# Performance work log

Hardware: AMD Instinct MI355X
Metric: run time of the kernel (lower is better)

Reference implementation:

```python
import jax, jax.numpy as jnp
import numpy as np

BATCH, N_IN, N_MID, N_OUT = 1048576, 64, 32, 10


def setup_inputs() -> dict:
    key = jax.random.key(0)
    k_x, k_w1, k_b1, k_w2, k_b2 = jax.random.split(key, 5)
    # scalar synapse weights k collectively form dense matrices; init like
    # Synapse.init_weight: uniform(-sqrt(1/fan_in), sqrt(1/fan_in))
    v1 = np.sqrt(1.0 / N_IN)
    v2 = np.sqrt(1.0 / N_MID)
    return {
        "x": jax.random.normal(k_x, (BATCH, N_IN), dtype=jnp.float32),
        "W1": jax.random.uniform(k_w1, (N_IN, N_MID), dtype=jnp.float32, minval=-v1, maxval=v1),
        "b1": jnp.zeros((N_MID,), dtype=jnp.float32),  # obtain_float_parameter inits to 0.0
        "W2": jax.random.uniform(k_w2, (N_MID, N_OUT), dtype=jnp.float32, minval=-v2, maxval=v2),
        "b2": jnp.zeros((N_OUT,), dtype=jnp.float32),
    }


def reference(x, W1, b1, W2, b2):
    # RegularNeuron: output = ReLU(b + sum_j k_j * input_j)  -> relu(x @ W1 + b1)
    h = jax.nn.relu(x @ W1 + b1)  # [batch, n_middle]
    # DestinationNeuron (no activation): y = b + sum_j k_j * h_j -> h @ W2 + b2
    y = h @ W2 + b2  # [batch, n_outputs]
    return y
```

## Files before the change

### kernel.cpp

```cpp
#include <hip/hip_runtime.h>


#define N_IN  64
#define N_MID 32
#define N_OUT 10

#define WAVES_PER_BLOCK 4
#define TILES_PER_WAVE  4
#define ROWS_PER_TILE   16
#define ROWS_PER_BLOCK  (WAVES_PER_BLOCK * TILES_PER_WAVE * ROWS_PER_TILE)
#define H_STRIDE        80

typedef short bf16x8 __attribute__((ext_vector_type(8)));
typedef float f32x4  __attribute__((ext_vector_type(4)));

static __device__ __forceinline__ short f2bf(float f) {
    __bf16 h = (__bf16)f;
    return __builtin_bit_cast(short, h);
}

static __device__ __forceinline__ unsigned pk2bf(float lo, float hi) {
    unsigned l = (unsigned short)__builtin_bit_cast(unsigned short, (__bf16)lo);
    unsigned h = (unsigned short)__builtin_bit_cast(unsigned short, (__bf16)hi);
    return (h << 16) | l;
}

__global__ __launch_bounds__(256)
void livenet_mfma(const float* __restrict__ x,
                  const float* __restrict__ W1,
                  const float* __restrict__ b1,
                  const float* __restrict__ W2,
                  const float* __restrict__ b2,
                  float* __restrict__ out,
                  int batch) {
    __shared__ unsigned char h_lds_all[WAVES_PER_BLOCK][ROWS_PER_TILE * H_STRIDE];

    const int lane = threadIdx.x & 63;
    const int wave = threadIdx.x >> 6;
    const int g    = lane >> 4;
    const int c    = lane & 15;

    unsigned char* h_lds = h_lds_all[wave];

    bf16x8 w1f[2][2];
    #pragma unroll
    for (int n = 0; n < 2; ++n)
        #pragma unroll
        for (int p = 0; p < 2; ++p)
            #pragma unroll
            for (int i = 0; i < 8; ++i) {
                int k = p * 32 + 8 * g + i;
                w1f[n][p][i] = f2bf(W1[k * N_MID + n * 16 + c]);
            }

    bf16x8 w2f;
    #pragma unroll
    for (int i = 0; i < 8; ++i) {
        int kpos = 8 * g + i;
        int col  = (kpos & 1) * 16 + (kpos >> 1);
        w2f[i] = (c < N_OUT) ? f2bf(W2[col * N_OUT + c]) : (short)0;
    }

    const float b1v0 = b1[c];
    const float b1v1 = b1[16 + c];
    const float b2v  = (c < N_OUT) ? b2[c] : 0.0f;

    const size_t wave_row0 = (size_t)blockIdx.x * ROWS_PER_BLOCK
                           + (size_t)wave * (TILES_PER_WAVE * ROWS_PER_TILE);
    const bool full = (wave_row0 + TILES_PER_WAVE * ROWS_PER_TILE) <= (size_t)batch;

    const float* xbase = x + (wave_row0 + (size_t)c) * N_IN + 8 * g;

    if (full) {
        float4 v0 = *(const float4*)(xbase + 0);
        float4 v1 = *(const float4*)(xbase + 4);
        float4 v2 = *(const float4*)(xbase + 32);
        float4 v3 = *(const float4*)(xbase + 36);

        #pragma unroll
        for (int t = 0; t < TILES_PER_WAVE; ++t) {
            float4 n0 = v0, n1 = v1, n2 = v2, n3 = v3;
            if (t + 1 < TILES_PER_WAVE) {
                const float* xp = xbase + (size_t)(t + 1) * ROWS_PER_TILE * N_IN;
                n0 = *(const float4*)(xp + 0);
                n1 = *(const float4*)(xp + 4);
                n2 = *(const float4*)(xp + 32);
                n3 = *(const float4*)(xp + 36);
            }

            bf16x8 a0, a1;
            a0[0] = f2bf(v0.x); a0[1] = f2bf(v0.y); a0[2] = f2bf(v0.z); a0[3] = f2bf(v0.w);
            a0[4] = f2bf(v1.x); a0[5] = f2bf(v1.y); a0[6] = f2bf(v1.z); a0[7] = f2bf(v1.w);
            a1[0] = f2bf(v2.x); a1[1] = f2bf(v2.y); a1[2] = f2bf(v2.z); a1[3] = f2bf(v2.w);
            a1[4] = f2bf(v3.x); a1[5] = f2bf(v3.y); a1[6] = f2bf(v3.z); a1[7] = f2bf(v3.w);

            f32x4 acc0 = {b1v0, b1v0, b1v0, b1v0};
            f32x4 acc1 = {b1v1, b1v1, b1v1, b1v1};
            acc0 = __builtin_amdgcn_mfma_f32_16x16x32_bf16(a0, w1f[0][0], acc0, 0, 0, 0);
            acc0 = __builtin_amdgcn_mfma_f32_16x16x32_bf16(a1, w1f[0][1], acc0, 0, 0, 0);
            acc1 = __builtin_amdgcn_mfma_f32_16x16x32_bf16(a0, w1f[1][0], acc1, 0, 0, 0);
            acc1 = __builtin_amdgcn_mfma_f32_16x16x32_bf16(a1, w1f[1][1], acc1, 0, 0, 0);

            #pragma unroll
            for (int r = 0; r < 4; ++r) {
                const int rowr = 4 * g + r;
                *(unsigned*)(h_lds + rowr * H_STRIDE + 4 * c) =
                    pk2bf(fmaxf(acc0[r], 0.0f), fmaxf(acc1[r], 0.0f));
            }
            __asm__ volatile("" ::: "memory");

            const bf16x8 hfrag = *(const bf16x8*)(h_lds + c * H_STRIDE + 16 * g);
            f32x4 acc2 = {b2v, b2v, b2v, b2v};
            acc2 = __builtin_amdgcn_mfma_f32_16x16x32_bf16(hfrag, w2f, acc2, 0, 0, 0);

            __asm__ volatile("" ::: "memory");

            if (c < N_OUT) {
                const size_t rb = wave_row0 + (size_t)t * ROWS_PER_TILE;
                float* op = out + (rb + 4 * g) * N_OUT + c;
                op[0 * N_OUT] = acc2[0];
                op[1 * N_OUT] = acc2[1];
                op[2 * N_OUT] = acc2[2];
                op[3 * N_OUT] = acc2[3];
            }

            v0 = n0; v1 = n1; v2 = n2; v3 = n3;
        }
    } else {
        for (int t = 0; t < TILES_PER_WAVE; ++t) {
            const size_t rb = wave_row0 + (size_t)t * ROWS_PER_TILE;
            if (rb + ROWS_PER_TILE > (size_t)batch) break;

            const float* xp = xbase + (size_t)t * ROWS_PER_TILE * N_IN;
            float4 v0 = *(const float4*)(xp + 0);
            float4 v1 = *(const float4*)(xp + 4);
            float4 v2 = *(const float4*)(xp + 32);
            float4 v3 = *(const float4*)(xp + 36);

            bf16x8 a0, a1;
            a0[0] = f2bf(v0.x); a0[1] = f2bf(v0.y); a0[2] = f2bf(v0.z); a0[3] = f2bf(v0.w);
            a0[4] = f2bf(v1.x); a0[5] = f2bf(v1.y); a0[6] = f2bf(v1.z); a0[7] = f2bf(v1.w);
            a1[0] = f2bf(v2.x); a1[1] = f2bf(v2.y); a1[2] = f2bf(v2.z); a1[3] = f2bf(v2.w);
            a1[4] = f2bf(v3.x); a1[5] = f2bf(v3.y); a1[6] = f2bf(v3.z); a1[7] = f2bf(v3.w);

            f32x4 acc0 = {b1v0, b1v0, b1v0, b1v0};
            f32x4 acc1 = {b1v1, b1v1, b1v1, b1v1};
            acc0 = __builtin_amdgcn_mfma_f32_16x16x32_bf16(a0, w1f[0][0], acc0, 0, 0, 0);
            acc0 = __builtin_amdgcn_mfma_f32_16x16x32_bf16(a1, w1f[0][1], acc0, 0, 0, 0);
            acc1 = __builtin_amdgcn_mfma_f32_16x16x32_bf16(a0, w1f[1][0], acc1, 0, 0, 0);
            acc1 = __builtin_amdgcn_mfma_f32_16x16x32_bf16(a1, w1f[1][1], acc1, 0, 0, 0);

            #pragma unroll
            for (int r = 0; r < 4; ++r) {
                const int rowr = 4 * g + r;
                *(unsigned*)(h_lds + rowr * H_STRIDE + 4 * c) =
                    pk2bf(fmaxf(acc0[r], 0.0f), fmaxf(acc1[r], 0.0f));
            }
            __asm__ volatile("" ::: "memory");

            const bf16x8 hfrag = *(const bf16x8*)(h_lds + c * H_STRIDE + 16 * g);
            f32x4 acc2 = {b2v, b2v, b2v, b2v};
            acc2 = __builtin_amdgcn_mfma_f32_16x16x32_bf16(hfrag, w2f, acc2, 0, 0, 0);

            __asm__ volatile("" ::: "memory");

            if (c < N_OUT) {
                float* op = out + (rb + 4 * g) * N_OUT + c;
                op[0 * N_OUT] = acc2[0];
                op[1 * N_OUT] = acc2[1];
                op[2 * N_OUT] = acc2[2];
                op[3 * N_OUT] = acc2[3];
            }
        }
    }
}

extern "C" void kernel_launch(void* const* d_in, const int* in_sizes, int n_in,
                              void* d_out, int out_size, void* d_ws, size_t ws_size,
                              hipStream_t stream) {
    const float* x  = (const float*)d_in[0];
    const float* W1 = (const float*)d_in[1];
    const float* b1 = (const float*)d_in[2];
    const float* W2 = (const float*)d_in[3];
    const float* b2 = (const float*)d_in[4];
    float* out = (float*)d_out;

    int batch = in_sizes[0] / N_IN;
    int grid  = (batch + ROWS_PER_BLOCK - 1) / ROWS_PER_BLOCK;
    livenet_mfma<<<grid, 256, 0, stream>>>(x, W1, b1, W2, b2, out, batch);
}
```

Before: 66.58 us.

## Stage x tiles into LDS with double-buffered direct global-to-LDS loads

In the full-tile path, each wave now streams its x tiles straight into a per-wave double buffer in LDS using global_load_lds. The LDS layout is XOR-swizzled so the fragment reads avoid bank conflicts, and manual vmcnt waits overlap the fetch of the next tile with compute on the current one. The goal is to cut the register cost of holding prefetched x and to make loads more fully coalesced. In exchange, each block now uses about 32 KB more LDS, which can lower occupancy, and correctness depends on the hand-written waitcnt accounting.

```diff
diff --git a/kernel.cpp b/kernel.cpp
--- a/kernel.cpp
+++ b/kernel.cpp
@@ -10,9 +10,14 @@
 #define ROWS_PER_TILE   16
 #define ROWS_PER_BLOCK  (WAVES_PER_BLOCK * TILES_PER_WAVE * ROWS_PER_TILE)
 #define H_STRIDE        80
+#define XTILE_BYTES     4096
+#define ROW_BYTES       256
 
 typedef short bf16x8 __attribute__((ext_vector_type(8)));
 typedef float f32x4  __attribute__((ext_vector_type(4)));
+
+typedef __attribute__((address_space(3))) unsigned char       lds_u8_as;
+typedef const __attribute__((address_space(1))) unsigned char glb_u8_as;
 
 static __device__ __forceinline__ short f2bf(float f) {
     __bf16 h = (__bf16)f;
@@ -33,14 +38,16 @@
                   const float* __restrict__ b2,
                   float* __restrict__ out,
                   int batch) {
-    __shared__ unsigned char h_lds_all[WAVES_PER_BLOCK][ROWS_PER_TILE * H_STRIDE];
+    __shared__ __align__(16) unsigned char xstage_all[WAVES_PER_BLOCK][2 * XTILE_BYTES];
+    __shared__ __align__(16) unsigned char h_lds_all[WAVES_PER_BLOCK][ROWS_PER_TILE * H_STRIDE];
 
     const int lane = threadIdx.x & 63;
     const int wave = threadIdx.x >> 6;
     const int g    = lane >> 4;
     const int c    = lane & 15;
 
-    unsigned char* h_lds = h_lds_all[wave];
+    unsigned char* xstage = xstage_all[wave];
+    unsigned char* h_lds  = h_lds_all[wave];
 
     bf16x8 w1f[2][2];
     #pragma unroll
@@ -65,34 +72,62 @@
     const float b1v1 = b1[16 + c];
     const float b2v  = (c < N_OUT) ? b2[c] : 0.0f;
 
+    const int r_lo    = lane >> 4;
+    const int mprime  = lane & 15;
+    unsigned srcoff[4];
+    #pragma unroll
+    for (int j = 0; j < 4; ++j) {
+        int r = 4 * j + r_lo;
+        srcoff[j] = (unsigned)(r * ROW_BYTES + 16 * (mprime ^ (r & 7)));
+    }
+
+    const int cw = c & 7;
+    const unsigned rd_a0lo = (unsigned)(c * ROW_BYTES + 16 * ((2 * g)     ^ cw));
+    const unsigned rd_a0hi = (unsigned)(c * ROW_BYTES + 16 * ((2 * g + 1) ^ cw));
+    const unsigned rd_a1lo = (unsigned)(c * ROW_BYTES + 16 * ((8 + 2 * g) ^ cw));
+    const unsigned rd_a1hi = (unsigned)(c * ROW_BYTES + 16 * ((9 + 2 * g) ^ cw));
+
     const size_t wave_row0 = (size_t)blockIdx.x * ROWS_PER_BLOCK
                            + (size_t)wave * (TILES_PER_WAVE * ROWS_PER_TILE);
     const bool full = (wave_row0 + TILES_PER_WAVE * ROWS_PER_TILE) <= (size_t)batch;
 
-    const float* xbase = x + (wave_row0 + (size_t)c) * N_IN + 8 * g;
-
     if (full) {
-        float4 v0 = *(const float4*)(xbase + 0);
-        float4 v1 = *(const float4*)(xbase + 4);
-        float4 v2 = *(const float4*)(xbase + 32);
-        float4 v3 = *(const float4*)(xbase + 36);
+        const unsigned char* xb = (const unsigned char*)x + wave_row0 * ROW_BYTES;
+
+        #pragma unroll
+        for (int j = 0; j < 4; ++j) {
+            __builtin_amdgcn_global_load_lds(
+                (glb_u8_as*)(xb + srcoff[j]),
+                (lds_u8_as*)(xstage + j * 1024), 16, 0, 0);
+        }
+        __asm__ volatile("s_waitcnt vmcnt(0)" ::: "memory");
+        __builtin_amdgcn_sched_barrier(0);
 
         #pragma unroll
         for (int t = 0; t < TILES_PER_WAVE; ++t) {
-            float4 n0 = v0, n1 = v1, n2 = v2, n3 = v3;
+            const unsigned char* xbuf = xstage + (t & 1) * XTILE_BYTES;
+
+            const float4 f0 = *(const float4*)(xbuf + rd_a0lo);
+            const float4 f1 = *(const float4*)(xbuf + rd_a0hi);
+            const float4 f2 = *(const float4*)(xbuf + rd_a1lo);
+            const float4 f3 = *(const float4*)(xbuf + rd_a1hi);
+
             if (t + 1 < TILES_PER_WAVE) {
-                const float* xp = xbase + (size_t)(t + 1) * ROWS_PER_TILE * N_IN;
-                n0 = *(const float4*)(xp + 0);
-                n1 = *(const float4*)(xp + 4);
-                n2 = *(const float4*)(xp + 32);
-                n3 = *(const float4*)(xp + 36);
+                const unsigned char* src = xb + (size_t)(t + 1) * XTILE_BYTES;
+                unsigned char* nbuf = xstage + ((t + 1) & 1) * XTILE_BYTES;
+                #pragma unroll
+                for (int j = 0; j < 4; ++j) {
+                    __builtin_amdgcn_global_load_lds(
+                        (glb_u8_as*)(src + srcoff[j]),
+                        (lds_u8_as*)(nbuf + j * 1024), 16, 0, 0);
+                }
             }
 
             bf16x8 a0, a1;
-            a0[0] = f2bf(v0.x); a0[1] = f2bf(v0.y); a0[2] = f2bf(v0.z); a0[3] = f2bf(v0.w);
-            a0[4] = f2bf(v1.x); a0[5] = f2bf(v1.y); a0[6] = f2bf(v1.z); a0[7] = f2bf(v1.w);
-            a1[0] = f2bf(v2.x); a1[1] = f2bf(v2.y); a1[2] = f2bf(v2.z); a1[3] = f2bf(v2.w);
-            a1[4] = f2bf(v3.x); a1[5] = f2bf(v3.y); a1[6] = f2bf(v3.z); a1[7] = f2bf(v3.w);
+            a0[0] = f2bf(f0.x); a0[1] = f2bf(f0.y); a0[2] = f2bf(f0.z); a0[3] = f2bf(f0.w);
+            a0[4] = f2bf(f1.x); a0[5] = f2bf(f1.y); a0[6] = f2bf(f1.z); a0[7] = f2bf(f1.w);
+            a1[0] = f2bf(f2.x); a1[1] = f2bf(f2.y); a1[2] = f2bf(f2.z); a1[3] = f2bf(f2.w);
+            a1[4] = f2bf(f3.x); a1[5] = f2bf(f3.y); a1[6] = f2bf(f3.z); a1[7] = f2bf(f3.w);
 
             f32x4 acc0 = {b1v0, b1v0, b1v0, b1v0};
             f32x4 acc1 = {b1v1, b1v1, b1v1, b1v1};
@@ -124,14 +159,17 @@
                 op[3 * N_OUT] = acc2[3];
             }
 
-            v0 = n0; v1 = n1; v2 = n2; v3 = n3;
+            if (t + 1 < TILES_PER_WAVE) {
+                __asm__ volatile("s_waitcnt vmcnt(4)" ::: "memory");
+                __builtin_amdgcn_sched_barrier(0);
+            }
         }
     } else {
         for (int t = 0; t < TILES_PER_WAVE; ++t) {
             const size_t rb = wave_row0 + (size_t)t * ROWS_PER_TILE;
             if (rb + ROWS_PER_TILE > (size_t)batch) break;
 
-            const float* xp = xbase + (size_t)t * ROWS_PER_TILE * N_IN;
+            const float* xp = x + (rb + (size_t)c) * N_IN + 8 * g;
             float4 v0 = *(const float4*)(xp + 0);
             float4 v1 = *(const float4*)(xp + 4);
             float4 v2 = *(const float4*)(xp + 32);
```

Result: faster. 62.49 us (-6.1%).
